# Performance work log

Hardware: AMD Instinct MI355X
Metric: run time of the kernel (lower is better)

## Reference

```python
import jax, jax.numpy as jnp
import numpy as np

EPSILON = 1e-05


def setup_inputs() -> dict:
    key = jax.random.key(0)
    k1, k2, k3 = jax.random.split(key, 3)
    B, T, D, K = 8, 4096, 256, 2048
    hidden_states = jax.random.normal(k1, (B, T, D), dtype=jnp.float32)
    embed_sum = jax.random.normal(k2, (K, D), dtype=jnp.float32)
    # cluster usage counts are positive in practice
    cluster_usage = jax.random.uniform(k3, (K,), dtype=jnp.float32) * 10.0 + 0.1
    return {
        "hidden_states": hidden_states,
        "embed_sum": embed_sum,
        "cluster_usage": cluster_usage,
    }


def reference(hidden_states, embed_sum, cluster_usage):
    # embed = embed_sum / clamp(cluster_usage, eps)   -> [K, D]
    embed = embed_sum / jnp.clip(cluster_usage, EPSILON, None)[:, None]

    shape = hidden_states.shape
    x = hidden_states.reshape(-1, shape[-1])  # [N, D]

    # squared L2 distances via norm expansion (argmin equals argmin of cdist p=2)
    x_sq = jnp.sum(x * x, axis=-1, keepdims=True)          # [N, 1]
    e_sq = jnp.sum(embed * embed, axis=-1)[None, :]         # [1, K]
    dots = jnp.einsum("nd,kd->nk", x, embed)               # [N, K]
    dists = x_sq - 2.0 * dots + e_sq                        # [N, K]

    embed_ind = jnp.argmin(dists, axis=-1)                 # [N]
    embed_ind = embed_ind.reshape(shape[:-1])              # [B, T]

    # decode: embedding lookup
    quantize = embed[embed_ind]                             # [B, T, D]
    return quantize, embed_ind
```

## Files before the change

### kernel.cpp

```cpp
#include <hip/hip_runtime.h>
#include <float.h>
#include <stdint.h>


#define EPSILON 1e-5f
#define DELTA   1e-3f

constexpr int D     = 256;
constexpr int K_TOT = 2048;

constexpr int BB0        = 65536;
constexpr int BBUF       = 4096;
constexpr int LDS_HALVES = BB0 + 2 * BBUF;
constexpr int DYN_LDS    = LDS_HALVES * 2;

typedef _Float16 half8v __attribute__((ext_vector_type(8)));
typedef _Float16 half4v __attribute__((ext_vector_type(4)));
typedef float    f32x4  __attribute__((ext_vector_type(4)));

__global__ void prep_kernel(const float* __restrict__ es,
                            const float* __restrict__ usage,
                            _Float16* __restrict__ ec,
                            float* __restrict__ esq,
                            int* __restrict__ counter) {
  const int bx   = blockIdx.x;
  const int t    = threadIdx.x;
  const int wid  = t >> 6;
  const int lane = t & 63;
  if (bx < K_TOT / 4) {
    const int k = bx * 4 + wid;
    const float u = fmaxf(usage[k], EPSILON);
    const float4 v = *(const float4*)(es + (size_t)k * D + lane * 4);
    float4 e;
    e.x = v.x / u; e.y = v.y / u; e.z = v.z / u; e.w = v.w / u;
    half4v h, lo;
    h.x = (_Float16)e.x; lo.x = (_Float16)(e.x - (float)h.x);
    h.y = (_Float16)e.y; lo.y = (_Float16)(e.y - (float)h.y);
    h.z = (_Float16)e.z; lo.z = (_Float16)(e.z - (float)h.z);
    h.w = (_Float16)e.w; lo.w = (_Float16)(e.w - (float)h.w);
    *(half4v*)(ec + (size_t)k * 512 + lane * 4)       = h;
    *(half4v*)(ec + (size_t)k * 512 + 256 + lane * 4) = lo;
    float s = e.x * e.x + e.y * e.y + e.z * e.z + e.w * e.w;
    #pragma unroll
    for (int m = 1; m < 64; m <<= 1) s += __shfl_xor(s, m, 64);
    if (lane == 0) esq[k] = s;
  } else {
    if (t == 0) *counter = 0;
  }
}

__global__ __launch_bounds__(512, 2)
void mm_kernel(const float* __restrict__ x, const _Float16* __restrict__ ec,
               const float* __restrict__ esq, float4* __restrict__ p4, int N) {
  extern __shared__ __align__(16) _Float16 lds[];
  const int t    = threadIdx.x;
  const int lane = t & 63;
  const int q    = lane >> 4;
  const int l15  = lane & 15;
  const int wid  = t >> 6;
  const int wn   = wid >> 1;
  const int wk   = wid & 1;
  const int n0   = blockIdx.x * 128;

  const int prow = t >> 2;
  const int pc   = t & 3;
  #pragma unroll
  for (int i = 0; i < 8; ++i) {
    const float* src = x + (size_t)(n0 + prow) * D + i * 32 + pc * 8;
    const float4 f0 = *(const float4*)src;
    const float4 f1 = *(const float4*)(src + 4);
    const float f[8] = {f0.x, f0.y, f0.z, f0.w, f1.x, f1.y, f1.z, f1.w};
    half8v hv, lv;
    #pragma unroll
    for (int e = 0; e < 8; ++e) {
      const _Float16 h = (_Float16)f[e];
      hv[e] = h;
      lv[e] = (_Float16)(f[e] - (float)h);
    }
    *(half8v*)&lds[i * 4096 + t * 8]       = hv;
    *(half8v*)&lds[(i + 8) * 4096 + t * 8] = lv;
  }

  const _Float16* pB0 = ec + (size_t)prow * 512 + pc * 8;
  __builtin_amdgcn_global_load_lds(
      (const __attribute__((address_space(1))) void*)pB0,
      (__attribute__((address_space(3))) void*)&lds[BB0 + t * 8], 16, 0, 0);
  __syncthreads();

  const int ah0 = (wn * 32 + l15) * 32 + q * 8;
  const int bh0 = (wk * 64 + l15) * 32 + q * 8;

  float rd0[2][4], rd1[2][4];
  int   ri0[2][4];
  #pragma unroll
  for (int mi = 0; mi < 2; ++mi)
    #pragma unroll
    for (int r = 0; r < 4; ++r) {
      rd0[mi][r] = FLT_MAX; rd1[mi][r] = FLT_MAX; ri0[mi][r] = 0x7fffffff;
    }

  int buf = 0;
  for (int kt = 0; kt < 16; ++kt) {
    const bool last_kt = (kt == 15);
    const _Float16* pk = pB0 + (size_t)kt * 65536;

    int   kc[4];
    float eqv[4];
    #pragma unroll
    for (int ni = 0; ni < 4; ++ni) {
      kc[ni]  = kt * 128 + wk * 64 + ni * 16 + l15;
      eqv[ni] = esq[kc[ni]];
    }

    f32x4 acc[2][4] = {};

    #pragma unroll
    for (int s = 0; s < 8; ++s) {
      __builtin_amdgcn_global_load_lds(
          (const __attribute__((address_space(1))) void*)(pk + (s + 1) * 32),
          (__attribute__((address_space(3))) void*)
              &lds[BB0 + (buf ^ 1) * BBUF + t * 8],
          16, 0, 0);
      half8v bf[4], ah[2], al[2];
      #pragma unroll
      for (int ni = 0; ni < 4; ++ni)
        bf[ni] = *(const half8v*)&lds[BB0 + buf * BBUF + bh0 + ni * 512];
      #pragma unroll
      for (int mi = 0; mi < 2; ++mi) {
        ah[mi] = *(const half8v*)&lds[s * 4096 + ah0 + mi * 512];
        al[mi] = *(const half8v*)&lds[(s + 8) * 4096 + ah0 + mi * 512];
      }
      #pragma unroll
      for (int mi = 0; mi < 2; ++mi)
        #pragma unroll
        for (int ni = 0; ni < 4; ++ni)
          acc[mi][ni] = __builtin_amdgcn_mfma_f32_16x16x32_f16(
              ah[mi], bf[ni], acc[mi][ni], 0, 0, 0);
      #pragma unroll
      for (int mi = 0; mi < 2; ++mi)
        #pragma unroll
        for (int ni = 0; ni < 4; ++ni)
          acc[mi][ni] = __builtin_amdgcn_mfma_f32_16x16x32_f16(
              al[mi], bf[ni], acc[mi][ni], 0, 0, 0);
      __syncthreads();
      buf ^= 1;
    }

    #pragma unroll
    for (int s = 8; s < 16; ++s) {
      if (!(last_kt && s == 15)) {
        const _Float16* np =
            (s == 15) ? (pB0 + (size_t)(kt + 1) * 65536) : (pk + (s + 1) * 32);
        __builtin_amdgcn_global_load_lds(
            (const __attribute__((address_space(1))) void*)np,
            (__attribute__((address_space(3))) void*)
                &lds[BB0 + (buf ^ 1) * BBUF + t * 8],
            16, 0, 0);
      }
      half8v bf[4], ah[2];
      #pragma unroll
      for (int ni = 0; ni < 4; ++ni)
        bf[ni] = *(const half8v*)&lds[BB0 + buf * BBUF + bh0 + ni * 512];
      #pragma unroll
      for (int mi = 0; mi < 2; ++mi)
        ah[mi] = *(const half8v*)&lds[(s - 8) * 4096 + ah0 + mi * 512];
      #pragma unroll
      for (int mi = 0; mi < 2; ++mi)
        #pragma unroll
        for (int ni = 0; ni < 4; ++ni)
          acc[mi][ni] = __builtin_amdgcn_mfma_f32_16x16x32_f16(
              ah[mi], bf[ni], acc[mi][ni], 0, 0, 0);
      __syncthreads();
      buf ^= 1;
    }

    #pragma unroll
    for (int ni = 0; ni < 4; ++ni) {
      #pragma unroll
      for (int mi = 0; mi < 2; ++mi) {
        #pragma unroll
        for (int r = 0; r < 4; ++r) {
          const float d = fmaf(-2.f, acc[mi][ni][r], eqv[ni]);
          if (d < rd0[mi][r]) {
            rd1[mi][r] = rd0[mi][r]; rd0[mi][r] = d; ri0[mi][r] = kc[ni];
          } else {
            rd1[mi][r] = fminf(rd1[mi][r], d);
          }
        }
      }
    }
  }

  #pragma unroll
  for (int mi = 0; mi < 2; ++mi) {
    #pragma unroll
    for (int r = 0; r < 4; ++r) {
      float d0 = rd0[mi][r], d1 = rd1[mi][r];
      int   i0 = ri0[mi][r];
      #pragma unroll
      for (int off = 1; off < 16; off <<= 1) {
        const float od0 = __shfl_xor(d0, off, 16);
        const int   oi0 = __shfl_xor(i0, off, 16);
        const float od1 = __shfl_xor(d1, off, 16);
        if (od0 < d0 || (od0 == d0 && oi0 < i0)) {
          d1 = fminf(d0, od1); d0 = od0; i0 = oi0;
        } else {
          d1 = fminf(d1, od0);
        }
      }
      if (l15 == mi * 8 + r) {
        const int n = n0 + wn * 32 + mi * 16 + q * 4 + r;
        p4[(size_t)n * 2 + wk] = make_float4(d0, __int_as_float(i0), d1, 0.f);
      }
    }
  }
}

__global__ void combine_kernel(const float4* __restrict__ p4,
                               const float* __restrict__ es,
                               const float* __restrict__ usage,
                               float* __restrict__ out_q,
                               float* __restrict__ out_i,
                               int* __restrict__ list,
                               int* __restrict__ counter,
                               unsigned long long* __restrict__ rmin, int N) {
  const int wid  = threadIdx.x >> 6;
  const int lane = threadIdx.x & 63;
  const int n    = blockIdx.x * 4 + wid;

  float d0 = FLT_MAX, d1 = FLT_MAX;
  int   i0 = 0x7fffffff;
  if (lane < 2) {
    const float4 pv = p4[(size_t)n * 2 + lane];
    d0 = pv.x; i0 = __float_as_int(pv.y); d1 = pv.z;
  }
  {
    const float od0 = __shfl_xor(d0, 1, 2);
    const int   oi0 = __shfl_xor(i0, 1, 2);
    const float od1 = __shfl_xor(d1, 1, 2);
    if (od0 < d0 || (od0 == d0 && oi0 < i0)) {
      d1 = fminf(d0, od1); d0 = od0; i0 = oi0;
    } else {
      d1 = fminf(d1, od0);
    }
  }
  const int   idx = __shfl(i0, 0, 64);
  const float g0  = __shfl(d0, 0, 64);
  const float g1  = __shfl(d1, 0, 64);

  const float u = fmaxf(usage[idx], EPSILON);
  const float4 e = *(const float4*)(es + (size_t)idx * D + lane * 4);
  float4 qv;
  qv.x = e.x / u; qv.y = e.y / u; qv.z = e.z / u; qv.w = e.w / u;
  *(float4*)(out_q + (size_t)n * D + lane * 4) = qv;
  if (lane == 0) {
    out_i[n] = (float)idx;
    if (g1 - g0 < DELTA) {
      rmin[n] = 0xFFFFFFFFFFFFFFFFull;
      const int pos = atomicAdd(counter, 1);
      list[pos] = n;
    }
  }
}

__global__ void repair_kernel(const float* __restrict__ x,
                              const float* __restrict__ es,
                              const float* __restrict__ usage,
                              const float* __restrict__ esq,
                              const int* __restrict__ list,
                              const int* __restrict__ counter,
                              unsigned long long* __restrict__ rmin) {
  __shared__ float xs[256];
  const int t    = threadIdx.x;
  const int w    = t >> 6;
  const int lane = t & 63;
  const int cnt  = *counter;
  const int kseg = blockIdx.x & 7;

  for (int j = blockIdx.x >> 3; j < cnt; j += 256) {
    const int n = list[j];
    __syncthreads();
    xs[t] = x[(size_t)n * D + t];
    __syncthreads();
    const float4 xv = *(const float4*)&xs[lane * 4];

    float bd = FLT_MAX;
    int   bi = 0x7fffffff;
    const int kb0 = kseg * 256 + w * 64;
    for (int kk = 0; kk < 64; kk += 4) {
      const int kbase = kb0 + kk;
      float pd[4];
      #pragma unroll
      for (int j2 = 0; j2 < 4; ++j2) {
        const int k = kbase + j2;
        const float rs = 1.0f / fmaxf(usage[k], EPSILON);
        const float4 e = *(const float4*)(es + (size_t)k * D + lane * 4);
        float p = xv.x * (e.x * rs);
        p = fmaf(xv.y, e.y * rs, p);
        p = fmaf(xv.z, e.z * rs, p);
        pd[j2] = fmaf(xv.w, e.w * rs, p);
      }
      #pragma unroll
      for (int off = 1; off < 64; off <<= 1) {
        pd[0] += __shfl_xor(pd[0], off, 64);
        pd[1] += __shfl_xor(pd[1], off, 64);
        pd[2] += __shfl_xor(pd[2], off, 64);
        pd[3] += __shfl_xor(pd[3], off, 64);
      }
      #pragma unroll
      for (int j2 = 0; j2 < 4; ++j2) {
        const float dst = fmaf(-2.f, pd[j2], esq[kbase + j2]);
        if (dst < bd) { bd = dst; bi = kbase + j2; }
      }
    }
    if (lane == 0) {
      uint32_t ub = __float_as_uint(bd);
      ub = (ub & 0x80000000u) ? ~ub : (ub | 0x80000000u);
      const unsigned long long pk =
          ((unsigned long long)ub << 32) | (unsigned)bi;
      atomicMin(&rmin[n], pk);
    }
  }
}

__global__ void repair2_kernel(const float* __restrict__ es,
                               const float* __restrict__ usage,
                               const int* __restrict__ list,
                               const int* __restrict__ counter,
                               const unsigned long long* __restrict__ rmin,
                               float* __restrict__ out_q,
                               float* __restrict__ out_i) {
  const int t   = threadIdx.x;
  const int cnt = *counter;
  for (int j = blockIdx.x; j < cnt; j += 1024) {
    const int n   = list[j];
    const int idx = (int)(rmin[n] & 0x7fffffffu);
    const float u = fmaxf(usage[idx], EPSILON);
    out_q[(size_t)n * D + t] = es[(size_t)idx * D + t] / u;
    if (t == 0) out_i[n] = (float)idx;
  }
}

constexpr int TN = 128;
constexpr int DC = 32;
constexpr int KS = 2;
constexpr int RS = 196;

__global__ void esq_kernel(const float* __restrict__ es,
                           const float* __restrict__ usage,
                           float* __restrict__ esq) {
  const int lane = threadIdx.x & 63;
  const int w    = threadIdx.x >> 6;
  const int k    = blockIdx.x * 4 + w;
  const float u  = fmaxf(usage[k], EPSILON);
  const float4 e = *(const float4*)(es + (size_t)k * D + lane * 4);
  const float a = e.x / u, b = e.y / u, c = e.z / u, d = e.w / u;
  float s = a * a + b * b + c * c + d * d;
  #pragma unroll
  for (int m = 1; m < 64; m <<= 1) s += __shfl_xor(s, m, 64);
  if (lane == 0) esq[k] = s;
}

__global__ __launch_bounds__(256, 2)
void dist_kernel(const float* __restrict__ x,
                 const float* __restrict__ es,
                 const float* __restrict__ usage,
                 const float* __restrict__ esq,
                 float* __restrict__ bestd,
                 int* __restrict__ besti, int N) {
  __shared__ float smX[DC * RS];
  __shared__ float smE[DC * RS];
  const int t    = threadIdx.x;
  const int tx   = t & 15;
  const int ty   = t >> 4;
  const int n0   = blockIdx.x * TN;
  const int half = blockIdx.y;

  float best[8];
  int   bidx[8];
  #pragma unroll
  for (int i = 0; i < 8; ++i) { best[i] = FLT_MAX; bidx[i] = 0; }

  for (int kt = 0; kt < (K_TOT / KS) / 128; ++kt) {
    const int k0 = half * (K_TOT / KS) + kt * 128;
    float acc[8][8];
    #pragma unroll
    for (int i = 0; i < 8; ++i)
      #pragma unroll
      for (int j = 0; j < 8; ++j) acc[i][j] = 0.f;

    for (int dc = 0; dc < D; dc += DC) {
      __syncthreads();
      #pragma unroll
      for (int i = 0; i < 4; ++i) {
        const int f    = i * 256 + t;
        const int row  = f >> 3;
        const int c4   = f & 7;
        const int pcol = row + ((row >> 3) << 2);
        const float4 xv =
            *(const float4*)(x + (size_t)(n0 + row) * D + dc + c4 * 4);
        smX[(c4 * 4 + 0) * RS + pcol] = xv.x;
        smX[(c4 * 4 + 1) * RS + pcol] = xv.y;
        smX[(c4 * 4 + 2) * RS + pcol] = xv.z;
        smX[(c4 * 4 + 3) * RS + pcol] = xv.w;
        const int kk = k0 + row;
        const float rs = 1.0f / fmaxf(usage[kk], EPSILON);
        const float4 ev =
            *(const float4*)(es + (size_t)kk * D + dc + c4 * 4);
        smE[(c4 * 4 + 0) * RS + pcol] = ev.x * rs;
        smE[(c4 * 4 + 1) * RS + pcol] = ev.y * rs;
        smE[(c4 * 4 + 2) * RS + pcol] = ev.z * rs;
        smE[(c4 * 4 + 3) * RS + pcol] = ev.w * rs;
      }
      __syncthreads();
      #pragma unroll 4
      for (int d = 0; d < DC; ++d) {
        const float* px = &smX[d * RS + ty * 12];
        const float* pe = &smE[d * RS + tx * 12];
        const float4 xa = *(const float4*)px;
        const float4 xb = *(const float4*)(px + 4);
        const float4 ea = *(const float4*)pe;
        const float4 eb = *(const float4*)(pe + 4);
        const float xr[8] = {xa.x, xa.y, xa.z, xa.w, xb.x, xb.y, xb.z, xb.w};
        const float er[8] = {ea.x, ea.y, ea.z, ea.w, eb.x, eb.y, eb.z, eb.w};
        #pragma unroll
        for (int i = 0; i < 8; ++i)
          #pragma unroll
          for (int jj = 0; jj < 8; ++jj)
            acc[i][jj] = fmaf(xr[i], er[jj], acc[i][jj]);
      }
    }
    #pragma unroll
    for (int jj = 0; jj < 8; ++jj) {
      const int k = k0 + tx * 8 + jj;
      const float eq = esq[k];
      #pragma unroll
      for (int i = 0; i < 8; ++i) {
        const float dst = fmaf(-2.0f, acc[i][jj], eq);
        if (dst < best[i]) { best[i] = dst; bidx[i] = k; }
      }
    }
  }
  __syncthreads();
  float* rd = smX;
  int*   ri = (int*)smE;
  #pragma unroll
  for (int i = 0; i < 8; ++i) {
    const int r = ty * 8 + i;
    rd[tx * TN + r] = best[i];
    ri[tx * TN + r] = bidx[i];
  }
  __syncthreads();
  for (int off = 8; off >= 1; off >>= 1) {
    if (tx < off) {
      #pragma unroll
      for (int i = 0; i < 8; ++i) {
        const int r = ty * 8 + i;
        const float da = rd[tx * TN + r], db = rd[(tx + off) * TN + r];
        const int   ia = ri[tx * TN + r], ib = ri[(tx + off) * TN + r];
        if (db < da || (db == da && ib < ia)) {
          rd[tx * TN + r] = db;
          ri[tx * TN + r] = ib;
        }
      }
    }
    __syncthreads();
  }
  if (tx == 0) {
    #pragma unroll
    for (int i = 0; i < 8; ++i) {
      const int r = ty * 8 + i;
      bestd[(size_t)half * N + n0 + r] = rd[r];
      besti[(size_t)half * N + n0 + r] = ri[r];
    }
  }
}

__global__ void gather_kernel(const float* __restrict__ es,
                              const float* __restrict__ usage,
                              const float* __restrict__ bestd,
                              const int* __restrict__ besti,
                              float* __restrict__ out_q,
                              float* __restrict__ out_i, int N) {
  const int w    = threadIdx.x >> 6;
  const int lane = threadIdx.x & 63;
  const int n    = blockIdx.x * 4 + w;
  const float d0 = bestd[n];
  const float d1 = bestd[(size_t)N + n];
  const int   i0 = besti[n];
  const int   i1 = besti[(size_t)N + n];
  const int idx = (d1 < d0) ? i1 : i0;
  const float u = fmaxf(usage[idx], EPSILON);
  const float4 e = *(const float4*)(es + (size_t)idx * D + lane * 4);
  float4 qv;
  qv.x = e.x / u; qv.y = e.y / u; qv.z = e.z / u; qv.w = e.w / u;
  *(float4*)(out_q + (size_t)n * D + lane * 4) = qv;
  if (lane == 0) out_i[n] = (float)idx;
}

extern "C" void kernel_launch(void* const* d_in, const int* in_sizes, int n_in,
                              void* d_out, int out_size, void* d_ws, size_t ws_size,
                              hipStream_t stream) {
  const float* x     = (const float*)d_in[0];
  const float* es    = (const float*)d_in[1];
  const float* usage = (const float*)d_in[2];
  const int N = in_sizes[0] / D;

  float* out_q = (float*)d_out;
  float* out_i = out_q + (size_t)N * D;

  const size_t EB = (size_t)K_TOT * 512 * 2;
  const size_t PB = (size_t)N * 2 * 16;
  const size_t off_p4   = EB;
  const size_t off_esq  = off_p4 + PB;
  const size_t off_list = off_esq + 8192;
  const size_t off_cnt  = off_list + (size_t)N * 4;
  const size_t off_rmin = off_cnt + 16;
  const size_t NEED     = off_rmin + (size_t)N * 8;

  char* wsb = (char*)d_ws;

  hipError_t attr_ok = hipFuncSetAttribute(
      (const void*)mm_kernel, hipFuncAttributeMaxDynamicSharedMemorySize,
      DYN_LDS);

  if (ws_size >= NEED && attr_ok == hipSuccess && (N % 128) == 0) {
    _Float16* ec   = (_Float16*)wsb;
    float4*   p4   = (float4*)(wsb + off_p4);
    float*    esq  = (float*)(wsb + off_esq);
    int*      list = (int*)(wsb + off_list);
    int*      cnt  = (int*)(wsb + off_cnt);
    unsigned long long* rmin = (unsigned long long*)(wsb + off_rmin);

    prep_kernel<<<K_TOT / 4 + 1, 256, 0, stream>>>(es, usage, ec, esq, cnt);
    mm_kernel<<<N / 128, 512, DYN_LDS, stream>>>(x, ec, esq, p4, N);
    combine_kernel<<<N / 4, 256, 0, stream>>>(p4, es, usage, out_q, out_i,
                                              list, cnt, rmin, N);
    repair_kernel<<<2048, 256, 0, stream>>>(x, es, usage, esq, list, cnt, rmin);
    repair2_kernel<<<1024, 256, 0, stream>>>(es, usage, list, cnt, rmin,
                                             out_q, out_i);
  } else {
    float* ws    = (float*)d_ws;
    float* esq   = ws;
    float* bestd = ws + K_TOT;
    int*   besti = (int*)(ws + K_TOT + (size_t)KS * N);
    esq_kernel<<<K_TOT / 4, 256, 0, stream>>>(es, usage, esq);
    dist_kernel<<<dim3(N / TN, KS), 256, 0, stream>>>(x, es, usage, esq,
                                                      bestd, besti, N);
    gather_kernel<<<N / 4, 256, 0, stream>>>(es, usage, bestd, besti,
                                             out_q, out_i, N);
  }
}
```

Measured before the change: 216.6 us.

## Fuse combine into mm kernel, swizzle LDS layout, keep A-high fragments in registers

Removes the separate combine kernel. The matmul kernel now merges the two K-half partial argmins through LDS and writes the gathered quantized rows, indices and repair-list entries directly. The p4 workspace round trip and one launch go away. It also XOR-swizzles the LDS layout of the x and codebook tiles to cut bank conflicts, and holds the high-half x fragments in registers (16 half8 vectors) for the whole K loop, which raises register pressure under launch_bounds(512,2).

New measurement: 210.1 us. 3.0% less time.

```diff
diff --git a/kernel.cpp b/kernel.cpp
--- a/kernel.cpp
+++ b/kernel.cpp
@@ -51,7 +51,11 @@
 
 __global__ __launch_bounds__(512, 2)
 void mm_kernel(const float* __restrict__ x, const _Float16* __restrict__ ec,
-               const float* __restrict__ esq, float4* __restrict__ p4, int N) {
+               const float* __restrict__ esq, const float* __restrict__ es,
+               const float* __restrict__ usage,
+               float* __restrict__ out_q, float* __restrict__ out_i,
+               int* __restrict__ list, int* __restrict__ counter,
+               unsigned long long* __restrict__ rmin, int N) {
   extern __shared__ __align__(16) _Float16 lds[];
   const int t    = threadIdx.x;
   const int lane = t & 63;
@@ -62,8 +66,21 @@
   const int wk   = wid & 1;
   const int n0   = blockIdx.x * 128;
 
-  const int prow = t >> 2;
-  const int pc   = t & 3;
+  {
+  }
+  const int pgr  = t & 63;
+  const int glog = pgr ^ ((pgr >> 3) & 3);
+  const int brow = (t >> 6) * 16 + (glog >> 2);
+  const int bch  = glog & 3;
+  const _Float16* pB0 = ec + (size_t)brow * 512 + bch * 8;
+
+  __builtin_amdgcn_global_load_lds(
+      (const __attribute__((address_space(1))) void*)pB0,
+      (__attribute__((address_space(3))) void*)&lds[BB0 + t * 8], 16, 0, 0);
+
+  const int prow  = t >> 2;
+  const int pc    = t & 3;
+  const int wbase = (t >> 6) * 512 + ((t & 63) ^ ((t >> 3) & 3)) * 8;
   #pragma unroll
   for (int i = 0; i < 8; ++i) {
     const float* src = x + (size_t)(n0 + prow) * D + i * 32 + pc * 8;
@@ -77,18 +94,20 @@
       hv[e] = h;
       lv[e] = (_Float16)(f[e] - (float)h);
     }
-    *(half8v*)&lds[i * 4096 + t * 8]       = hv;
-    *(half8v*)&lds[(i + 8) * 4096 + t * 8] = lv;
-  }
-
-  const _Float16* pB0 = ec + (size_t)prow * 512 + pc * 8;
-  __builtin_amdgcn_global_load_lds(
-      (const __attribute__((address_space(1))) void*)pB0,
-      (__attribute__((address_space(3))) void*)&lds[BB0 + t * 8], 16, 0, 0);
+    *(half8v*)&lds[i * 4096 + wbase]       = hv;
+    *(half8v*)&lds[(i + 8) * 4096 + wbase] = lv;
+  }
   __syncthreads();
 
-  const int ah0 = (wn * 32 + l15) * 32 + q * 8;
-  const int bh0 = (wk * 64 + l15) * 32 + q * 8;
+  const int gA = l15 * 4 + q;
+  const int sp = (gA ^ ((l15 >> 1) & 3)) * 8;
+
+  half8v ahr[8][2];
+  #pragma unroll
+  for (int s = 0; s < 8; ++s)
+    #pragma unroll
+    for (int mi = 0; mi < 2; ++mi)
+      ahr[s][mi] = *(const half8v*)&lds[s * 4096 + wn * 1024 + mi * 512 + sp];
 
   float rd0[2][4], rd1[2][4];
   int   ri0[2][4];
@@ -115,39 +134,7 @@
     f32x4 acc[2][4] = {};
 
     #pragma unroll
-    for (int s = 0; s < 8; ++s) {
-      __builtin_amdgcn_global_load_lds(
-          (const __attribute__((address_space(1))) void*)(pk + (s + 1) * 32),
-          (__attribute__((address_space(3))) void*)
-              &lds[BB0 + (buf ^ 1) * BBUF + t * 8],
-          16, 0, 0);
-      half8v bf[4], ah[2], al[2];
-      #pragma unroll
-      for (int ni = 0; ni < 4; ++ni)
-        bf[ni] = *(const half8v*)&lds[BB0 + buf * BBUF + bh0 + ni * 512];
-      #pragma unroll
-      for (int mi = 0; mi < 2; ++mi) {
-        ah[mi] = *(const half8v*)&lds[s * 4096 + ah0 + mi * 512];
-        al[mi] = *(const half8v*)&lds[(s + 8) * 4096 + ah0 + mi * 512];
-      }
-      #pragma unroll
-      for (int mi = 0; mi < 2; ++mi)
-        #pragma unroll
-        for (int ni = 0; ni < 4; ++ni)
-          acc[mi][ni] = __builtin_amdgcn_mfma_f32_16x16x32_f16(
-              ah[mi], bf[ni], acc[mi][ni], 0, 0, 0);
-      #pragma unroll
-      for (int mi = 0; mi < 2; ++mi)
-        #pragma unroll
-        for (int ni = 0; ni < 4; ++ni)
-          acc[mi][ni] = __builtin_amdgcn_mfma_f32_16x16x32_f16(
-              al[mi], bf[ni], acc[mi][ni], 0, 0, 0);
-      __syncthreads();
-      buf ^= 1;
-    }
-
-    #pragma unroll
-    for (int s = 8; s < 16; ++s) {
+    for (int s = 0; s < 16; ++s) {
       if (!(last_kt && s == 15)) {
         const _Float16* np =
             (s == 15) ? (pB0 + (size_t)(kt + 1) * 65536) : (pk + (s + 1) * 32);
@@ -157,19 +144,37 @@
                 &lds[BB0 + (buf ^ 1) * BBUF + t * 8],
             16, 0, 0);
       }
-      half8v bf[4], ah[2];
+      half8v bf[4];
       #pragma unroll
       for (int ni = 0; ni < 4; ++ni)
-        bf[ni] = *(const half8v*)&lds[BB0 + buf * BBUF + bh0 + ni * 512];
-      #pragma unroll
-      for (int mi = 0; mi < 2; ++mi)
-        ah[mi] = *(const half8v*)&lds[(s - 8) * 4096 + ah0 + mi * 512];
-      #pragma unroll
-      for (int mi = 0; mi < 2; ++mi)
+        bf[ni] = *(const half8v*)
+            &lds[BB0 + buf * BBUF + wk * 2048 + ni * 512 + sp];
+      if (s < 8) {
+        half8v al[2];
         #pragma unroll
-        for (int ni = 0; ni < 4; ++ni)
-          acc[mi][ni] = __builtin_amdgcn_mfma_f32_16x16x32_f16(
-              ah[mi], bf[ni], acc[mi][ni], 0, 0, 0);
+        for (int mi = 0; mi < 2; ++mi)
+          al[mi] = *(const half8v*)
+              &lds[(s + 8) * 4096 + wn * 1024 + mi * 512 + sp];
+        #pragma unroll
+        for (int mi = 0; mi < 2; ++mi)
+          #pragma unroll
+          for (int ni = 0; ni < 4; ++ni)
+            acc[mi][ni] = __builtin_amdgcn_mfma_f32_16x16x32_f16(
+                ahr[s][mi], bf[ni], acc[mi][ni], 0, 0, 0);
+        #pragma unroll
+        for (int mi = 0; mi < 2; ++mi)
+          #pragma unroll
+          for (int ni = 0; ni < 4; ++ni)
+            acc[mi][ni] = __builtin_amdgcn_mfma_f32_16x16x32_f16(
+                al[mi], bf[ni], acc[mi][ni], 0, 0, 0);
+      } else {
+        #pragma unroll
+        for (int mi = 0; mi < 2; ++mi)
+          #pragma unroll
+          for (int ni = 0; ni < 4; ++ni)
+            acc[mi][ni] = __builtin_amdgcn_mfma_f32_16x16x32_f16(
+                ahr[s - 8][mi], bf[ni], acc[mi][ni], 0, 0, 0);
+      }
       __syncthreads();
       buf ^= 1;
     }
@@ -191,6 +196,7 @@
     }
   }
 
+  float* ex = (float*)lds;
   #pragma unroll
   for (int mi = 0; mi < 2; ++mi) {
     #pragma unroll
@@ -209,56 +215,43 @@
         }
       }
       if (l15 == mi * 8 + r) {
-        const int n = n0 + wn * 32 + mi * 16 + q * 4 + r;
-        p4[(size_t)n * 2 + wk] = make_float4(d0, __int_as_float(i0), d1, 0.f);
-      }
-    }
-  }
-}
-
-__global__ void combine_kernel(const float4* __restrict__ p4,
-                               const float* __restrict__ es,
-                               const float* __restrict__ usage,
-                               float* __restrict__ out_q,
-                               float* __restrict__ out_i,
-                               int* __restrict__ list,
-                               int* __restrict__ counter,
-                               unsigned long long* __restrict__ rmin, int N) {
-  const int wid  = threadIdx.x >> 6;
-  const int lane = threadIdx.x & 63;
-  const int n    = blockIdx.x * 4 + wid;
-
-  float d0 = FLT_MAX, d1 = FLT_MAX;
-  int   i0 = 0x7fffffff;
-  if (lane < 2) {
-    const float4 pv = p4[(size_t)n * 2 + lane];
-    d0 = pv.x; i0 = __float_as_int(pv.y); d1 = pv.z;
-  }
+        const int row = wn * 32 + mi * 16 + q * 4 + r;
+        *(float4*)&ex[(row * 2 + wk) * 4] =
+            make_float4(d0, __int_as_float(i0), d1, 0.f);
+      }
+    }
+  }
+  __syncthreads();
+
   {
-    const float od0 = __shfl_xor(d0, 1, 2);
-    const int   oi0 = __shfl_xor(i0, 1, 2);
-    const float od1 = __shfl_xor(d1, 1, 2);
-    if (od0 < d0 || (od0 == d0 && oi0 < i0)) {
-      d1 = fminf(d0, od1); d0 = od0; i0 = oi0;
+    const int row = t >> 2;
+    const int seg = t & 3;
+    const float4 a = *(const float4*)&ex[(row * 2 + 0) * 4];
+    const float4 b = *(const float4*)&ex[(row * 2 + 1) * 4];
+    float d0, d1; int i0;
+    const int ia = __float_as_int(a.y), ib = __float_as_int(b.y);
+    if (b.x < a.x || (b.x == a.x && ib < ia)) {
+      d0 = b.x; i0 = ib; d1 = fminf(a.x, b.z);
     } else {
-      d1 = fminf(d1, od0);
-    }
-  }
-  const int   idx = __shfl(i0, 0, 64);
-  const float g0  = __shfl(d0, 0, 64);
-  const float g1  = __shfl(d1, 0, 64);
-
-  const float u = fmaxf(usage[idx], EPSILON);
-  const float4 e = *(const float4*)(es + (size_t)idx * D + lane * 4);
-  float4 qv;
-  qv.x = e.x / u; qv.y = e.y / u; qv.z = e.z / u; qv.w = e.w / u;
-  *(float4*)(out_q + (size_t)n * D + lane * 4) = qv;
-  if (lane == 0) {
-    out_i[n] = (float)idx;
-    if (g1 - g0 < DELTA) {
-      rmin[n] = 0xFFFFFFFFFFFFFFFFull;
-      const int pos = atomicAdd(counter, 1);
-      list[pos] = n;
+      d0 = a.x; i0 = ia; d1 = fminf(a.z, b.x);
+    }
+    const int n = n0 + row;
+    const float u  = fmaxf(usage[i0], EPSILON);
+    const float4* src = (const float4*)(es + (size_t)i0 * D);
+    float4*       dst = (float4*)(out_q + (size_t)n * D);
+    #pragma unroll
+    for (int i = 0; i < 16; ++i) {
+      const int j = i * 4 + seg;
+      const float4 e = src[j];
+      dst[j] = make_float4(e.x / u, e.y / u, e.z / u, e.w / u);
+    }
+    if (seg == 0) {
+      out_i[n] = (float)i0;
+      if (d1 - d0 < DELTA) {
+        rmin[n] = 0xFFFFFFFFFFFFFFFFull;
+        const int pos = atomicAdd(counter, 1);
+        list[pos] = n;
+      }
     }
   }
 }
@@ -510,9 +503,7 @@
   float* out_i = out_q + (size_t)N * D;
 
   const size_t EB = (size_t)K_TOT * 512 * 2;
-  const size_t PB = (size_t)N * 2 * 16;
-  const size_t off_p4   = EB;
-  const size_t off_esq  = off_p4 + PB;
+  const size_t off_esq  = EB;
   const size_t off_list = off_esq + 8192;
   const size_t off_cnt  = off_list + (size_t)N * 4;
   const size_t off_rmin = off_cnt + 16;
@@ -526,16 +517,15 @@
 
   if (ws_size >= NEED && attr_ok == hipSuccess && (N % 128) == 0) {
     _Float16* ec   = (_Float16*)wsb;
-    float4*   p4   = (float4*)(wsb + off_p4);
     float*    esq  = (float*)(wsb + off_esq);
     int*      list = (int*)(wsb + off_list);
     int*      cnt  = (int*)(wsb + off_cnt);
     unsigned long long* rmin = (unsigned long long*)(wsb + off_rmin);
 
     prep_kernel<<<K_TOT / 4 + 1, 256, 0, stream>>>(es, usage, ec, esq, cnt);
-    mm_kernel<<<N / 128, 512, DYN_LDS, stream>>>(x, ec, esq, p4, N);
-    combine_kernel<<<N / 4, 256, 0, stream>>>(p4, es, usage, out_q, out_i,
-                                              list, cnt, rmin, N);
+    mm_kernel<<<N / 128, 512, DYN_LDS, stream>>>(x, ec, esq, es, usage,
+                                                 out_q, out_i, list, cnt,
+                                                 rmin, N);
     repair_kernel<<<2048, 256, 0, stream>>>(x, es, usage, esq, list, cnt, rmin);
     repair2_kernel<<<1024, 256, 0, stream>>>(es, usage, list, cnt, rmin,
                                              out_q, out_i);
```
